# Performance work log

Hardware: AMD Instinct MI355X
Metric: run time of the kernel (lower is better)

## Reference

```python
import jax, jax.numpy as jnp
import numpy as np

HID = 4096      # hidden_size
H = 32          # num_attention_heads
K = 8           # num_key_value_heads
D = HID // H    # head_dim = 128
G = H // K      # q heads per kv group = 4
INTER = 14336   # intermediate_size
T = 2048        # tokens (prefill)
EPS = 1e-5
THETA = 1000000.0


def setup_inputs() -> dict:
    key = jax.random.key(0)
    ks = jax.random.split(key, 9)
    s = 0.02
    return {
        "hidden_states": jax.random.normal(ks[0], (T, HID), jnp.float32),
        "position_ids": jnp.arange(T, dtype=jnp.int64),
        "wqkv": jax.random.normal(ks[1], ((H + 2 * K) * D, HID), jnp.float32) * s,
        "wo": jax.random.normal(ks[2], (HID, HID), jnp.float32) * s,
        "w1": jax.random.normal(ks[3], (INTER, HID), jnp.float32) * s,  # gate
        "w3": jax.random.normal(ks[4], (INTER, HID), jnp.float32) * s,  # up
        "w2": jax.random.normal(ks[5], (HID, INTER), jnp.float32) * s,  # down
        "attn_norm_w": jnp.ones((HID,), jnp.float32),
        "ffn_norm_w": jnp.ones((HID,), jnp.float32),
    }


def _rmsnorm(x, w):
    var = jnp.mean(jnp.square(x), axis=-1, keepdims=True)
    return x * jax.lax.rsqrt(var + EPS) * w


def _rope(x, cos, sin):
    # non-interleaved (half-split) rotation; x: [T, h, D], cos/sin: [T, 1, D//2]
    x1, x2 = x[..., : D // 2], x[..., D // 2 :]
    return jnp.concatenate([x1 * cos - x2 * sin, x2 * cos + x1 * sin], axis=-1)


def _attention(x, position_ids, wqkv, wo):
    t = x.shape[0]
    qkv = x @ wqkv.T  # [T, (H+2K)*D]
    q = qkv[:, : H * D].reshape(t, H, D)
    k = qkv[:, H * D : (H + K) * D].reshape(t, K, D)
    v = qkv[:, (H + K) * D :].reshape(t, K, D)

    inv_freq = 1.0 / (THETA ** (jnp.arange(0, D, 2, dtype=jnp.float32) / D))
    freqs = position_ids.astype(jnp.float32)[:, None] * inv_freq  # [T, D//2]
    cos = jnp.cos(freqs)[:, None, :]
    sin = jnp.sin(freqs)[:, None, :]
    q = _rope(q, cos, sin)
    k = _rope(k, cos, sin)

    # grouped-query attention: [T, K, G, D] queries vs [T, K, D] keys
    qg = q.reshape(t, K, G, D)
    scale = 1.0 / jnp.sqrt(jnp.float32(D))
    scores = jnp.einsum("tkgd,skd->kgts", qg, k) * scale  # [K, G, T, T]
    causal = jnp.tril(jnp.ones((t, t), dtype=bool))
    scores = jnp.where(causal, scores, jnp.finfo(scores.dtype).min)
    probs = jax.nn.softmax(scores, axis=-1)
    out = jnp.einsum("kgts,skd->tkgd", probs, v).reshape(t, H * D)
    return out @ wo.T


def _mlp(x, w1, w3, w2):
    return (jax.nn.silu(x @ w1.T) * (x @ w3.T)) @ w2.T


def reference(hidden_states, position_ids, wqkv, wo, w1, w3, w2, attn_norm_w, ffn_norm_w):
    h = hidden_states + _attention(_rmsnorm(hidden_states, attn_norm_w), position_ids, wqkv, wo)
    return h + _mlp(_rmsnorm(h, ffn_norm_w), w1, w3, w2)
```

## Files before the change

kernel.cpp:

```cpp
#include <hip/hip_runtime.h>
#include <stdint.h>

#define T_SEQ 2048
#define HIDN  4096
#define NH    32
#define NKV   8
#define DH    128
#define INTER 14336
#define QKV_N 6144
#define EPSR  1e-5f
#define SCALE 0.08838834764831845f
#define KVB   64

typedef __bf16 bf16x8 __attribute__((ext_vector_type(8)));
typedef float  f32x4  __attribute__((ext_vector_type(4)));

__device__ __forceinline__ f32x4 mfma16(bf16x8 a, bf16x8 b, f32x4 c) {
  return __builtin_amdgcn_mfma_f32_16x16x32_bf16(a, b, c, 0, 0, 0);
}

__device__ __forceinline__ void glds16(const void* g, void* l) {
  __builtin_amdgcn_global_load_lds(
      (__attribute__((address_space(1))) void*)g,
      (__attribute__((address_space(3))) void*)l,
      16, 0, 0);
}

__global__ __launch_bounds__(256) void cvt_bf16_kernel(
    const float* __restrict__ src, __bf16* __restrict__ dst, long n) {
  long stride = (long)gridDim.x * 256 * 8;
  for (long i = ((long)blockIdx.x * 256 + threadIdx.x) * 8; i < n; i += stride) {
    float4 a = *(const float4*)(src + i);
    float4 b = *(const float4*)(src + i + 4);
    bf16x8 o;
    o[0]=(__bf16)a.x; o[1]=(__bf16)a.y; o[2]=(__bf16)a.z; o[3]=(__bf16)a.w;
    o[4]=(__bf16)b.x; o[5]=(__bf16)b.y; o[6]=(__bf16)b.z; o[7]=(__bf16)b.w;
    *(bf16x8*)(dst + i) = o;
  }
}

__global__ __launch_bounds__(256) void cvt_w13_kernel(
    const float* __restrict__ w1, const float* __restrict__ w3,
    __bf16* __restrict__ dst) {
  for (int c = blockIdx.x; c < 2 * INTER; c += gridDim.x) {
    int tau = c >> 8, j2 = c & 255;
    int wn = j2 >> 7, j = j2 & 127, nt = j >> 4, k16 = j & 15;
    const float* src = (nt < 4 ? w1 : w3) +
        (size_t)(tau * 128 + wn * 64 + (nt & 3) * 16 + k16) * HIDN;
    __bf16* d = dst + (size_t)c * HIDN;
    int i = threadIdx.x * 16;
    float4 a = *(const float4*)(src + i);
    float4 b = *(const float4*)(src + i + 4);
    float4 e = *(const float4*)(src + i + 8);
    float4 f = *(const float4*)(src + i + 12);
    bf16x8 o0, o1;
    o0[0]=(__bf16)a.x; o0[1]=(__bf16)a.y; o0[2]=(__bf16)a.z; o0[3]=(__bf16)a.w;
    o0[4]=(__bf16)b.x; o0[5]=(__bf16)b.y; o0[6]=(__bf16)b.z; o0[7]=(__bf16)b.w;
    o1[0]=(__bf16)e.x; o1[1]=(__bf16)e.y; o1[2]=(__bf16)e.z; o1[3]=(__bf16)e.w;
    o1[4]=(__bf16)f.x; o1[5]=(__bf16)f.y; o1[6]=(__bf16)f.z; o1[7]=(__bf16)f.w;
    *(bf16x8*)(d + i) = o0;
    *(bf16x8*)(d + i + 8) = o1;
  }
}

__global__ __launch_bounds__(256) void rmsnorm_kernel(
    const float* __restrict__ x, const float* __restrict__ w,
    __bf16* __restrict__ y) {
  const int row = blockIdx.x, tid = threadIdx.x;
  const float* xr = x + (size_t)row * HIDN + tid * 16;
  float4 v0 = ((const float4*)xr)[0];
  float4 v1 = ((const float4*)xr)[1];
  float4 v2 = ((const float4*)xr)[2];
  float4 v3 = ((const float4*)xr)[3];
  float ss = v0.x*v0.x + v0.y*v0.y + v0.z*v0.z + v0.w*v0.w
           + v1.x*v1.x + v1.y*v1.y + v1.z*v1.z + v1.w*v1.w
           + v2.x*v2.x + v2.y*v2.y + v2.z*v2.z + v2.w*v2.w
           + v3.x*v3.x + v3.y*v3.y + v3.z*v3.z + v3.w*v3.w;
  #pragma unroll
  for (int off = 32; off >= 1; off >>= 1) ss += __shfl_xor(ss, off, 64);
  __shared__ float red[4];
  if ((tid & 63) == 0) red[tid >> 6] = ss;
  __syncthreads();
  float rn = rsqrtf((red[0] + red[1] + red[2] + red[3]) * (1.0f / HIDN) + EPSR);
  const float* wr = w + tid * 16;
  #pragma unroll
  for (int h = 0; h < 2; h++) {
    float4 a = ((const float4*)xr)[h*2], b = ((const float4*)xr)[h*2+1];
    float4 wa = ((const float4*)wr)[h*2], wb = ((const float4*)wr)[h*2+1];
    bf16x8 o;
    o[0]=(__bf16)(a.x*rn*wa.x); o[1]=(__bf16)(a.y*rn*wa.y);
    o[2]=(__bf16)(a.z*rn*wa.z); o[3]=(__bf16)(a.w*rn*wa.w);
    o[4]=(__bf16)(b.x*rn*wb.x); o[5]=(__bf16)(b.y*rn*wb.y);
    o[6]=(__bf16)(b.z*rn*wb.z); o[7]=(__bf16)(b.w*rn*wb.w);
    *(bf16x8*)(y + (size_t)row * HIDN + tid * 16 + h * 8) = o;
  }
}

__global__ __launch_bounds__(256) void add3_rms_kernel(
    const float* __restrict__ p, const float* __restrict__ resid,
    const float* __restrict__ w, float* __restrict__ hout,
    __bf16* __restrict__ xn) {
  const int row = blockIdx.x, tid = threadIdx.x;
  const size_t base = (size_t)row * HIDN + tid * 16;
  const size_t half = (size_t)T_SEQ * HIDN;
  float h[16];
  float ss = 0.f;
  #pragma unroll
  for (int q = 0; q < 4; q++) {
    float4 a = *(const float4*)(p + base + q * 4);
    float4 b = *(const float4*)(p + half + base + q * 4);
    float4 c = *(const float4*)(resid + base + q * 4);
    h[q*4+0] = a.x + b.x + c.x; h[q*4+1] = a.y + b.y + c.y;
    h[q*4+2] = a.z + b.z + c.z; h[q*4+3] = a.w + b.w + c.w;
    ss += h[q*4]*h[q*4] + h[q*4+1]*h[q*4+1] + h[q*4+2]*h[q*4+2] + h[q*4+3]*h[q*4+3];
    *(float4*)(hout + base + q * 4) = *(float4*)&h[q*4];
  }
  #pragma unroll
  for (int off = 32; off >= 1; off >>= 1) ss += __shfl_xor(ss, off, 64);
  __shared__ float red[4];
  if ((tid & 63) == 0) red[tid >> 6] = ss;
  __syncthreads();
  float rn = rsqrtf((red[0] + red[1] + red[2] + red[3]) * (1.0f / HIDN) + EPSR);
  #pragma unroll
  for (int hb = 0; hb < 2; hb++) {
    bf16x8 o;
    #pragma unroll
    for (int e = 0; e < 8; e++) {
      float wv = w[tid * 16 + hb * 8 + e];
      o[e] = (__bf16)(h[hb*8+e] * rn * wv);
    }
    *(bf16x8*)(xn + base + hb * 8) = o;
  }
}

template<int EPI>
__global__ __launch_bounds__(256, 2) void gemm128_kernel(
    const __bf16* __restrict__ A, const __bf16* __restrict__ B,
    void* __restrict__ Cout, int M, int N, int Kfull, int KZ, int Nout) {
  extern __shared__ __align__(16) char smem[];
  const int tid = threadIdx.x;
  const int lane = tid & 63;
  const int wv = tid >> 6;
  const int wm = wv >> 1;
  const int wn = wv & 1;
  const int lr = lane & 15, ql = lane >> 4;

  const int gx = gridDim.x, gy = gridDim.y;
  const int nwg = gx * gy;
  const int orig = blockIdx.y * gx + blockIdx.x;
  const int cpx = nwg >> 3;
  const int swz = (orig & 7) * cpx + (orig >> 3);
  const int by = swz % gy, bx = swz / gy;
  const int m0 = by * 128, n0 = bx * 256;
  const int kbase = blockIdx.z * KZ;
  const int NT = KZ >> 5;

  const char* gS[6]; int lD[6];
  #pragma unroll
  for (int j = 0; j < 6; j++) {
    int u = (j < 2) ? (j * 256 + tid) : (512 + (j - 2) * 256 + tid);
    if (j < 2) {
      int row = u >> 2;
      int s = (u & 3) ^ ((row >> 1) & 3);
      gS[j] = (const char*)(A + (size_t)(m0 + row) * Kfull + kbase) + s * 16;
      lD[j] = u * 16;
    } else {
      int u2 = u - 512;
      int row = u2 >> 2;
      int s = (u2 & 3) ^ ((row >> 1) & 3);
      gS[j] = (const char*)(B + (size_t)(n0 + row) * Kfull + kbase) + s * 16;
      lD[j] = 8192 + u2 * 16;
    }
  }

  const int sA = ql ^ ((lr >> 1) & 3);
  int aoff[4], boff[8];
  #pragma unroll
  for (int mt = 0; mt < 4; mt++) aoff[mt] = (wm * 64 + mt * 16 + lr) * 64 + sA * 16;
  #pragma unroll
  for (int nt = 0; nt < 8; nt++) boff[nt] = 8192 + (wn * 128 + nt * 16 + lr) * 64 + sA * 16;

#define STAGE(t, b) do {                                           \
    const size_t _o = (size_t)(t) * 64;                            \
    char* _d = smem + (b) * 24576;                                 \
    glds16(gS[0] + _o, _d + lD[0]); glds16(gS[1] + _o, _d + lD[1]);\
    glds16(gS[2] + _o, _d + lD[2]); glds16(gS[3] + _o, _d + lD[3]);\
    glds16(gS[4] + _o, _d + lD[4]); glds16(gS[5] + _o, _d + lD[5]);\
  } while (0)
#define LOADFRAGS(b) do {                                          \
    const char* _p = smem + (b) * 24576;                           \
    _Pragma("unroll") for (int _m = 0; _m < 4; _m++)               \
      af[_m] = *(const bf16x8*)(_p + aoff[_m]);                    \
    _Pragma("unroll") for (int _n = 0; _n < 8; _n++)               \
      bf[_n] = *(const bf16x8*)(_p + boff[_n]);                    \
  } while (0)
#define WAITK() do { asm volatile("s_waitcnt lgkmcnt(0)" ::: "memory"); \
    __builtin_amdgcn_sched_barrier(0); } while (0)
#define MFMA32() do {                                              \
    __builtin_amdgcn_s_setprio(1);                                 \
    _Pragma("unroll") for (int _m = 0; _m < 4; _m++)               \
      _Pragma("unroll") for (int _n = 0; _n < 8; _n++)             \
        acc[_m][_n] = mfma16(af[_m], bf[_n], acc[_m][_n]);         \
    __builtin_amdgcn_s_setprio(0);                                 \
  } while (0)
#define INC3(v) v = (v == 2) ? 0 : v + 1

  f32x4 acc[4][8] = {};
  bf16x8 af[4], bf[8];

  STAGE(0, 0); STAGE(1, 1);
  int bufi = 0, sbufi = 2;
  for (int t = 0; t < NT - 2; ++t) {
    asm volatile("s_waitcnt vmcnt(6)" ::: "memory");
    __builtin_amdgcn_s_barrier();
    LOADFRAGS(bufi);
    STAGE(t + 2, sbufi);
    WAITK(); MFMA32();
    INC3(bufi); INC3(sbufi);
  }
  asm volatile("s_waitcnt vmcnt(6)" ::: "memory");
  __builtin_amdgcn_s_barrier();
  LOADFRAGS(bufi);
  WAITK(); MFMA32();
  INC3(bufi);
  asm volatile("s_waitcnt vmcnt(0)" ::: "memory");
  __builtin_amdgcn_s_barrier();
  LOADFRAGS(bufi);
  WAITK(); MFMA32();

#undef STAGE
#undef LOADFRAGS
#undef WAITK
#undef MFMA32
#undef INC3

  #pragma unroll
  for (int mt = 0; mt < 4; mt++) {
    #pragma unroll
    for (int r = 0; r < 4; r++) {
      int rr = m0 + wm * 64 + mt * 16 + ql * 4 + r;
      if (EPI == 2) {
        #pragma unroll
        for (int nt = 0; nt < 4; nt++) {
          float u = acc[mt][nt][r];
          float v = acc[mt][nt + 4][r];
          float g = u / (1.0f + __expf(-u)) * v;
          int cc = (n0 >> 1) + wn * 64 + nt * 16 + lr;
          ((__bf16*)Cout)[(size_t)rr * Nout + cc] = (__bf16)g;
        }
      } else {
        #pragma unroll
        for (int nt = 0; nt < 8; nt++) {
          int cc = n0 + wn * 128 + nt * 16 + lr;
          size_t ix = (size_t)rr * N + cc;
          float val = acc[mt][nt][r];
          if (EPI == 0) ((float*)Cout)[(size_t)blockIdx.z * M * N + ix] = val;
          else          ((__bf16*)Cout)[ix] = (__bf16)val;
        }
      }
    }
  }
}

__global__ __launch_bounds__(256) void add3_kernel(
    const float* __restrict__ p, const float* __restrict__ r,
    float* __restrict__ o, long n) {
  long stride = (long)gridDim.x * 1024;
  for (long i = ((long)blockIdx.x * 256 + threadIdx.x) * 4; i < n; i += stride) {
    float4 a = *(const float4*)(p + i);
    float4 b = *(const float4*)(p + n + i);
    float4 c = *(const float4*)(r + i);
    float4 o4;
    o4.x = a.x + b.x + c.x; o4.y = a.y + b.y + c.y;
    o4.z = a.z + b.z + c.z; o4.w = a.w + b.w + c.w;
    *(float4*)(o + i) = o4;
  }
}

__global__ __launch_bounds__(256) void rope_kernel(
    const __bf16* __restrict__ qkv, __bf16* __restrict__ q_r,
    __bf16* __restrict__ k_r) {
  const int t = blockIdx.x, tid = threadIdx.x;
  __shared__ float cs[64], sn[64];
  if (tid < 64) {
    float inv = exp2f(-(float)tid * (19.931568569324174f / 64.0f));
    float f = (float)t * inv;
    cs[tid] = cosf(f);
    sn[tid] = sinf(f);
  }
  __syncthreads();
  const __bf16* row = qkv + (size_t)t * QKV_N;
  for (int it = tid; it < 40 * 64; it += 256) {
    int hh = it >> 6, i = it & 63;
    float x1 = (float)row[hh * 128 + i];
    float x2 = (float)row[hh * 128 + 64 + i];
    float c = cs[i], s = sn[i];
    float o1 = x1 * c - x2 * s;
    float o2 = x2 * c + x1 * s;
    if (hh < NH) {
      __bf16* qo = q_r + (size_t)t * HIDN + hh * 128;
      qo[i] = (__bf16)o1;
      qo[64 + i] = (__bf16)o2;
    } else {
      __bf16* ko = k_r + (size_t)t * (NKV * DH) + (hh - NH) * 128;
      ko[i] = (__bf16)o1;
      ko[64 + i] = (__bf16)o2;
    }
  }
}

__global__ __launch_bounds__(256) void vtrans_kernel(
    const __bf16* __restrict__ qkv, __bf16* __restrict__ v_t) {
  __shared__ __bf16 tile[64][136];
  const int tid = threadIdx.x;
  const int t0 = blockIdx.x * 64, kh = blockIdx.y;
  #pragma unroll
  for (int i = 0; i < 4; i++) {
    int u = i * 256 + tid;
    int row = u >> 4, c = (u & 15) * 8;
    *(bf16x8*)&tile[row][c] =
        *(const bf16x8*)(qkv + (size_t)(t0 + row) * QKV_N + (NH + NKV) * DH + kh * DH + c);
  }
  __syncthreads();
  const int d = tid & 127, th = (tid >> 7) * 32;
  #pragma unroll
  for (int j = 0; j < 4; j++) {
    int t = th + j * 8;
    bf16x8 o;
    #pragma unroll
    for (int e = 0; e < 8; e++) o[e] = tile[t + e][d];
    *(bf16x8*)(v_t + ((size_t)kh * DH + d) * T_SEQ + t0 + t) = o;
  }
}

__global__ __launch_bounds__(256) void attn_kernel(
    const __bf16* __restrict__ q_r, const __bf16* __restrict__ k_r,
    const __bf16* __restrict__ v_t, __bf16* __restrict__ attn_o) {
  __shared__ __align__(16) __bf16 Ks[KVB * 128];
  __shared__ __align__(16) __bf16 Vs[128 * KVB];
  __shared__ __align__(16) __bf16 Pl[4 * 16 * KVB];

  const int tid = threadIdx.x;
  const int lane = tid & 63, wv = tid >> 6;
  const int lr = lane & 15, g = lane >> 4;
  const int qt = gridDim.x - 1 - blockIdx.x;
  const int h = blockIdx.y;
  const int kh = h >> 2;
  const int q0b = qt * 64;
  const int q0w = q0b + wv * 16;

  bf16x8 qf[4];
  {
    const __bf16* qp = q_r + (size_t)(q0w + lr) * HIDN + h * DH + g * 8;
    #pragma unroll
    for (int kk = 0; kk < 4; kk++) qf[kk] = *(const bf16x8*)(qp + kk * 32);
  }

  f32x4 o[8] = {};
  float mrun[4] = {-1e30f, -1e30f, -1e30f, -1e30f};
  float lrun[4] = {0.f, 0.f, 0.f, 0.f};
  char* PlW = (char*)Pl + wv * 2048;

  for (int kv0 = 0; kv0 < q0b + KVB; kv0 += KVB) {
    __syncthreads();
    #pragma unroll
    for (int i = 0; i < 4; i++) {
      int u = i * 256 + tid;
      int row = u >> 4;
      int cb = ((u & 15) * 16) ^ ((row & 7) << 4);
      glds16((const char*)(k_r + (size_t)(kv0 + row) * (NKV * DH) + kh * DH) + cb,
             (char*)Ks + u * 16);
    }
    #pragma unroll
    for (int i = 0; i < 4; i++) {
      int u = i * 256 + tid;
      int row = u >> 3;
      int cb = ((u & 7) * 16) ^ ((row & 7) << 4);
      glds16((const char*)(v_t + ((size_t)kh * DH + row) * T_SEQ + kv0) + cb,
             (char*)Vs + u * 16);
    }
    __syncthreads();

    if (q0w + 15 >= kv0) {
      f32x4 s[4] = {};
      #pragma unroll
      for (int kk = 0; kk < 4; kk++) {
        #pragma unroll
        for (int jt = 0; jt < 4; jt++) {
          int krow = jt * 16 + lr;
          int cb = (kk * 64 + g * 16) ^ ((krow & 7) << 4);
          bf16x8 kf = *(const bf16x8*)((char*)Ks + krow * 256 + cb);
          s[jt] = mfma16(qf[kk], kf, s[jt]);
        }
      }
      const bool need_mask = (kv0 + KVB - 1) > q0w;
      #pragma unroll
      for (int r = 0; r < 4; r++) {
        int qpos = q0w + g * 4 + r;
        int prow = g * 4 + r;
        float p[4];
        #pragma unroll
        for (int jt = 0; jt < 4; jt++) {
          float v = s[jt][r] * SCALE;
          if (need_mask && (kv0 + jt * 16 + lr > qpos)) v = -1e30f;
          p[jt] = v;
        }
        float mx = fmaxf(fmaxf(p[0], p[1]), fmaxf(p[2], p[3]));
        #pragma unroll
        for (int off = 1; off < 16; off <<= 1) mx = fmaxf(mx, __shfl_xor(mx, off, 64));
        float mn = fmaxf(mrun[r], mx);
        float corr = __expf(mrun[r] - mn);
        mrun[r] = mn;
        float ps = 0.f;
        #pragma unroll
        for (int jt = 0; jt < 4; jt++) {
          p[jt] = __expf(p[jt] - mn);
          ps += p[jt];
          int cbyte = ((jt * 16 + lr) * 2) ^ ((prow & 7) << 4);
          *(__bf16*)(PlW + prow * 128 + cbyte) = (__bf16)p[jt];
        }
        #pragma unroll
        for (int off = 1; off < 16; off <<= 1) ps += __shfl_xor(ps, off, 64);
        lrun[r] = lrun[r] * corr + ps;
        #pragma unroll
        for (int nt = 0; nt < 8; nt++) o[nt][r] *= corr;
      }
      bf16x8 pa[2];
      #pragma unroll
      for (int ks = 0; ks < 2; ks++)
        pa[ks] = *(const bf16x8*)(PlW + lr * 128 + ((g * 16 + ks * 64) ^ ((lr & 7) << 4)));
      #pragma unroll
      for (int nt = 0; nt < 8; nt++) {
        #pragma unroll
        for (int ks = 0; ks < 2; ks++) {
          int vrow = nt * 16 + lr;
          int cb = (ks * 64 + g * 16) ^ ((vrow & 7) << 4);
          bf16x8 vf = *(const bf16x8*)((char*)Vs + vrow * 128 + cb);
          o[nt] = mfma16(pa[ks], vf, o[nt]);
        }
      }
    }
  }

  #pragma unroll
  for (int nt = 0; nt < 8; nt++) {
    #pragma unroll
    for (int r = 0; r < 4; r++) {
      int qrow = q0w + g * 4 + r;
      int d = nt * 16 + lr;
      attn_o[(size_t)qrow * HIDN + h * DH + d] = (__bf16)(o[nt][r] / lrun[r]);
    }
  }
}

extern "C" void kernel_launch(void* const* d_in, const int* in_sizes, int n_in,
                              void* d_out, int out_size, void* d_ws, size_t ws_size,
                              hipStream_t stream) {
  const float* hidden = (const float*)d_in[0];
  const float* wqkv = (const float*)d_in[2];
  const float* wo   = (const float*)d_in[3];
  const float* w1   = (const float*)d_in[4];
  const float* w3   = (const float*)d_in[5];
  const float* w2   = (const float*)d_in[6];
  const float* anw  = (const float*)d_in[7];
  const float* fnw  = (const float*)d_in[8];

  char* ws = (char*)d_ws;
  const size_t SZ_XN   = (size_t)T_SEQ * HIDN * 2;
  const size_t SZ_QKV  = (size_t)T_SEQ * QKV_N * 2;
  const size_t SZ_KR   = (size_t)T_SEQ * NKV * DH * 2;
  const size_t SZ_H    = (size_t)T_SEQ * HIDN * 4;
  const size_t SZ_UV   = (size_t)T_SEQ * INTER * 2;

  const size_t W_QKV = (size_t)QKV_N * HIDN * 2;
  const size_t W_O   = (size_t)HIDN * HIDN * 2;
  const size_t W_I   = (size_t)INTER * HIDN * 2;
  const size_t W_TOTAL = W_QKV + W_O + 3 * W_I;

  char* act = ws + W_TOTAL;

  __bf16* xn1    = (__bf16*)(act);
  __bf16* qkv    = (__bf16*)(act + SZ_XN);
  __bf16* q_r    = (__bf16*)(act + SZ_XN + SZ_QKV);
  __bf16* gbuf   = (__bf16*)(act);
  __bf16* k_r    = (__bf16*)(act + SZ_UV);
  __bf16* attn_o = (__bf16*)(act + SZ_UV + SZ_KR);
  float*  hbuf   = (float*) (act + SZ_UV + SZ_KR + SZ_XN);
  __bf16* v_t    = (__bf16*)(act + SZ_UV + SZ_KR + SZ_XN);
  __bf16* xn2    = (__bf16*)(act + SZ_UV + SZ_KR + SZ_XN + SZ_H);
  float*  pbuf   = (float*)(act + SZ_UV + SZ_KR + SZ_XN + SZ_H + SZ_XN);

  __bf16* wqkv_b = (__bf16*)(ws);
  __bf16* wo_b   = (__bf16*)(ws + W_QKV);
  __bf16* w13_b  = (__bf16*)(ws + W_QKV + W_O);
  __bf16* w2_b   = (__bf16*)(ws + W_QKV + W_O + 2 * W_I);

  const int LDS_BYTES = 73728;
  hipFuncSetAttribute((const void*)gemm128_kernel<0>,
                      hipFuncAttributeMaxDynamicSharedMemorySize, LDS_BYTES);
  hipFuncSetAttribute((const void*)gemm128_kernel<1>,
                      hipFuncAttributeMaxDynamicSharedMemorySize, LDS_BYTES);
  hipFuncSetAttribute((const void*)gemm128_kernel<2>,
                      hipFuncAttributeMaxDynamicSharedMemorySize, LDS_BYTES);

  cvt_bf16_kernel<<<2048, 256, 0, stream>>>(wqkv, wqkv_b, (long)QKV_N * HIDN);
  cvt_bf16_kernel<<<2048, 256, 0, stream>>>(wo,   wo_b,   (long)HIDN * HIDN);
  cvt_w13_kernel<<<2048, 256, 0, stream>>>(w1, w3, w13_b);
  cvt_bf16_kernel<<<2048, 256, 0, stream>>>(w2,   w2_b,   (long)HIDN * INTER);

  rmsnorm_kernel<<<T_SEQ, 256, 0, stream>>>(hidden, anw, xn1);
  gemm128_kernel<1><<<dim3(QKV_N / 256, T_SEQ / 128, 1), 256, LDS_BYTES, stream>>>(
      xn1, wqkv_b, qkv, T_SEQ, QKV_N, HIDN, HIDN, QKV_N);
  rope_kernel<<<T_SEQ, 256, 0, stream>>>(qkv, q_r, k_r);
  vtrans_kernel<<<dim3(T_SEQ / 64, NKV), 256, 0, stream>>>(qkv, v_t);
  attn_kernel<<<dim3(T_SEQ / 64, NH), 256, 0, stream>>>(q_r, k_r, v_t, attn_o);
  gemm128_kernel<0><<<dim3(HIDN / 256, T_SEQ / 128, 2), 256, LDS_BYTES, stream>>>(
      attn_o, wo_b, pbuf, T_SEQ, HIDN, HIDN, HIDN / 2, HIDN);
  add3_rms_kernel<<<T_SEQ, 256, 0, stream>>>(pbuf, hidden, fnw, hbuf, xn2);
  gemm128_kernel<2><<<dim3(2 * INTER / 256, T_SEQ / 128, 1), 256, LDS_BYTES, stream>>>(
      xn2, w13_b, gbuf, T_SEQ, 2 * INTER, HIDN, HIDN, INTER);
  gemm128_kernel<0><<<dim3(HIDN / 256, T_SEQ / 128, 2), 256, LDS_BYTES, stream>>>(
      gbuf, w2_b, pbuf, T_SEQ, HIDN, INTER, INTER / 2, HIDN);
  add3_kernel<<<2048, 256, 0, stream>>>(pbuf, hbuf, (float*)d_out, (long)T_SEQ * HIDN);
}
```

Before: 1.367 ms.

## Fuse fp32-to-bf16 weight conversion into GEMM B-tile loading

Removes the separate weight conversion kernels and the bf16 weight workspace. Each GEMM now loads fp32 weight rows into registers, converts them to bf16 and writes them swizzled into LDS with double buffering. The A operand keeps async global-to-LDS loads. This trades the standalone conversion passes for doubled B-operand bytes per tile, extra register pressure and VALU conversion work inside the GEMM main loop.

```diff
diff --git a/kernel.cpp b/kernel.cpp
--- a/kernel.cpp
+++ b/kernel.cpp
@@ -24,43 +24,6 @@
       (__attribute__((address_space(1))) void*)g,
       (__attribute__((address_space(3))) void*)l,
       16, 0, 0);
-}
-
-__global__ __launch_bounds__(256) void cvt_bf16_kernel(
-    const float* __restrict__ src, __bf16* __restrict__ dst, long n) {
-  long stride = (long)gridDim.x * 256 * 8;
-  for (long i = ((long)blockIdx.x * 256 + threadIdx.x) * 8; i < n; i += stride) {
-    float4 a = *(const float4*)(src + i);
-    float4 b = *(const float4*)(src + i + 4);
-    bf16x8 o;
-    o[0]=(__bf16)a.x; o[1]=(__bf16)a.y; o[2]=(__bf16)a.z; o[3]=(__bf16)a.w;
-    o[4]=(__bf16)b.x; o[5]=(__bf16)b.y; o[6]=(__bf16)b.z; o[7]=(__bf16)b.w;
-    *(bf16x8*)(dst + i) = o;
-  }
-}
-
-__global__ __launch_bounds__(256) void cvt_w13_kernel(
-    const float* __restrict__ w1, const float* __restrict__ w3,
-    __bf16* __restrict__ dst) {
-  for (int c = blockIdx.x; c < 2 * INTER; c += gridDim.x) {
-    int tau = c >> 8, j2 = c & 255;
-    int wn = j2 >> 7, j = j2 & 127, nt = j >> 4, k16 = j & 15;
-    const float* src = (nt < 4 ? w1 : w3) +
-        (size_t)(tau * 128 + wn * 64 + (nt & 3) * 16 + k16) * HIDN;
-    __bf16* d = dst + (size_t)c * HIDN;
-    int i = threadIdx.x * 16;
-    float4 a = *(const float4*)(src + i);
-    float4 b = *(const float4*)(src + i + 4);
-    float4 e = *(const float4*)(src + i + 8);
-    float4 f = *(const float4*)(src + i + 12);
-    bf16x8 o0, o1;
-    o0[0]=(__bf16)a.x; o0[1]=(__bf16)a.y; o0[2]=(__bf16)a.z; o0[3]=(__bf16)a.w;
-    o0[4]=(__bf16)b.x; o0[5]=(__bf16)b.y; o0[6]=(__bf16)b.z; o0[7]=(__bf16)b.w;
-    o1[0]=(__bf16)e.x; o1[1]=(__bf16)e.y; o1[2]=(__bf16)e.z; o1[3]=(__bf16)e.w;
-    o1[4]=(__bf16)f.x; o1[5]=(__bf16)f.y; o1[6]=(__bf16)f.z; o1[7]=(__bf16)f.w;
-    *(bf16x8*)(d + i) = o0;
-    *(bf16x8*)(d + i + 8) = o1;
-  }
 }
 
 __global__ __launch_bounds__(256) void rmsnorm_kernel(
@@ -134,9 +97,10 @@
 }
 
 template<int EPI>
-__global__ __launch_bounds__(256, 2) void gemm128_kernel(
-    const __bf16* __restrict__ A, const __bf16* __restrict__ B,
-    void* __restrict__ Cout, int M, int N, int Kfull, int KZ, int Nout) {
+__global__ __launch_bounds__(256, 2) void gemmf_kernel(
+    const __bf16* __restrict__ A, const float* __restrict__ B1,
+    const float* __restrict__ B2, void* __restrict__ Cout,
+    int M, int N, int Kfull, int KZ, int Nout) {
   extern __shared__ __align__(16) char smem[];
   const int tid = threadIdx.x;
   const int lane = tid & 63;
@@ -155,47 +119,64 @@
   const int kbase = blockIdx.z * KZ;
   const int NT = KZ >> 5;
 
-  const char* gS[6]; int lD[6];
-  #pragma unroll
-  for (int j = 0; j < 6; j++) {
-    int u = (j < 2) ? (j * 256 + tid) : (512 + (j - 2) * 256 + tid);
-    if (j < 2) {
-      int row = u >> 2;
-      int s = (u & 3) ^ ((row >> 1) & 3);
-      gS[j] = (const char*)(A + (size_t)(m0 + row) * Kfull + kbase) + s * 16;
-      lD[j] = u * 16;
-    } else {
-      int u2 = u - 512;
-      int row = u2 >> 2;
-      int s = (u2 & 3) ^ ((row >> 1) & 3);
-      gS[j] = (const char*)(B + (size_t)(n0 + row) * Kfull + kbase) + s * 16;
-      lD[j] = 8192 + u2 * 16;
-    }
-  }
+  const char* aSrc[2]; int aDst[2];
+  #pragma unroll
+  for (int j = 0; j < 2; j++) {
+    int u = j * 256 + tid;
+    int row = u >> 2;
+    int s = (u & 3) ^ ((row >> 1) & 3);
+    aSrc[j] = (const char*)(A + (size_t)(m0 + row) * Kfull + kbase) + s * 16;
+    aDst[j] = u * 16;
+  }
+
+  const float* bptr;
+  if (EPI == 2) {
+    int r = tid;
+    const float* wsel = ((r >> 6) & 1) ? B2 : B1;
+    int grow = (n0 >> 1) + ((r >> 7) << 6) + (r & 63);
+    bptr = wsel + (size_t)grow * Kfull + kbase;
+  } else {
+    bptr = B1 + (size_t)(n0 + tid) * Kfull + kbase;
+  }
+  int wof[4];
+  #pragma unroll
+  for (int s = 0; s < 4; s++) wof[s] = (s ^ ((tid >> 1) & 3)) * 16;
 
   const int sA = ql ^ ((lr >> 1) & 3);
   int aoff[4], boff[8];
   #pragma unroll
   for (int mt = 0; mt < 4; mt++) aoff[mt] = (wm * 64 + mt * 16 + lr) * 64 + sA * 16;
   #pragma unroll
-  for (int nt = 0; nt < 8; nt++) boff[nt] = 8192 + (wn * 128 + nt * 16 + lr) * 64 + sA * 16;
-
-#define STAGE(t, b) do {                                           \
-    const size_t _o = (size_t)(t) * 64;                            \
-    char* _d = smem + (b) * 24576;                                 \
-    glds16(gS[0] + _o, _d + lD[0]); glds16(gS[1] + _o, _d + lD[1]);\
-    glds16(gS[2] + _o, _d + lD[2]); glds16(gS[3] + _o, _d + lD[3]);\
-    glds16(gS[4] + _o, _d + lD[4]); glds16(gS[5] + _o, _d + lD[5]);\
+  for (int nt = 0; nt < 8; nt++) boff[nt] = (wn * 128 + nt * 16 + lr) * 64 + sA * 16;
+
+#define BUFA(i) (smem + (i) * 8192)
+#define BUFB(i) (smem + 24576 + (i) * 16384)
+#define STAGE_A(t, bi) do {                                        \
+    glds16(aSrc[0] + (size_t)(t) * 64, BUFA(bi) + aDst[0]);        \
+    glds16(aSrc[1] + (size_t)(t) * 64, BUFA(bi) + aDst[1]);        \
   } while (0)
-#define LOADFRAGS(b) do {                                          \
-    const char* _p = smem + (b) * 24576;                           \
+#define LOAD_B(t) do {                                             \
+    _Pragma("unroll") for (int _j = 0; _j < 8; _j++)               \
+      breg[_j] = ((const float4*)bptr)[(size_t)(t) * 8 + _j];      \
+  } while (0)
+#define WRITE_B(bi) do {                                           \
+    char* _wb = BUFB(bi) + tid * 64;                               \
+    _Pragma("unroll") for (int _s = 0; _s < 4; _s++) {             \
+      bf16x8 _o;                                                   \
+      _o[0]=(__bf16)breg[2*_s].x;   _o[1]=(__bf16)breg[2*_s].y;    \
+      _o[2]=(__bf16)breg[2*_s].z;   _o[3]=(__bf16)breg[2*_s].w;    \
+      _o[4]=(__bf16)breg[2*_s+1].x; _o[5]=(__bf16)breg[2*_s+1].y;  \
+      _o[6]=(__bf16)breg[2*_s+1].z; _o[7]=(__bf16)breg[2*_s+1].w;  \
+      *(bf16x8*)(_wb + wof[_s]) = _o;                              \
+    }                                                              \
+  } while (0)
+#define LOADFRAGS(ai, bi) do {                                     \
+    const char* _pa = BUFA(ai); const char* _pb = BUFB(bi);        \
     _Pragma("unroll") for (int _m = 0; _m < 4; _m++)               \
-      af[_m] = *(const bf16x8*)(_p + aoff[_m]);                    \
+      af[_m] = *(const bf16x8*)(_pa + aoff[_m]);                   \
     _Pragma("unroll") for (int _n = 0; _n < 8; _n++)               \
-      bf[_n] = *(const bf16x8*)(_p + boff[_n]);                    \
+      bf[_n] = *(const bf16x8*)(_pb + boff[_n]);                   \
   } while (0)
-#define WAITK() do { asm volatile("s_waitcnt lgkmcnt(0)" ::: "memory"); \
-    __builtin_amdgcn_sched_barrier(0); } while (0)
 #define MFMA32() do {                                              \
     __builtin_amdgcn_s_setprio(1);                                 \
     _Pragma("unroll") for (int _m = 0; _m < 4; _m++)               \
@@ -204,35 +185,42 @@
     __builtin_amdgcn_s_setprio(0);                                 \
   } while (0)
 #define INC3(v) v = (v == 2) ? 0 : v + 1
+#define CLAMP(t) ((t) < NT ? (t) : NT - 1)
 
   f32x4 acc[4][8] = {};
   bf16x8 af[4], bf[8];
-
-  STAGE(0, 0); STAGE(1, 1);
-  int bufi = 0, sbufi = 2;
-  for (int t = 0; t < NT - 2; ++t) {
-    asm volatile("s_waitcnt vmcnt(6)" ::: "memory");
+  float4 breg[8];
+
+  LOAD_B(0);
+  STAGE_A(0, 0); STAGE_A(1, 1);
+  WRITE_B(0);
+  LOAD_B(CLAMP(1));
+  asm volatile("s_waitcnt vmcnt(8)" ::: "memory");
+  asm volatile("s_waitcnt lgkmcnt(0)" ::: "memory");
+
+  int ai = 0, asi = 2;
+  for (int t = 0; t < NT; ++t) {
+    asm volatile("s_waitcnt vmcnt(10)" ::: "memory");
     __builtin_amdgcn_s_barrier();
-    LOADFRAGS(bufi);
-    STAGE(t + 2, sbufi);
-    WAITK(); MFMA32();
-    INC3(bufi); INC3(sbufi);
-  }
-  asm volatile("s_waitcnt vmcnt(6)" ::: "memory");
-  __builtin_amdgcn_s_barrier();
-  LOADFRAGS(bufi);
-  WAITK(); MFMA32();
-  INC3(bufi);
-  asm volatile("s_waitcnt vmcnt(0)" ::: "memory");
-  __builtin_amdgcn_s_barrier();
-  LOADFRAGS(bufi);
-  WAITK(); MFMA32();
-
-#undef STAGE
+    LOADFRAGS(ai, t & 1);
+    STAGE_A(CLAMP(t + 2), asi);
+    WRITE_B((t + 1) & 1);
+    LOAD_B(CLAMP(t + 2));
+    asm volatile("s_waitcnt lgkmcnt(0)" ::: "memory");
+    __builtin_amdgcn_sched_barrier(0);
+    MFMA32();
+    INC3(ai); INC3(asi);
+  }
+
+#undef BUFA
+#undef BUFB
+#undef STAGE_A
+#undef LOAD_B
+#undef WRITE_B
 #undef LOADFRAGS
-#undef WAITK
 #undef MFMA32
 #undef INC3
+#undef CLAMP
 
   #pragma unroll
   for (int mt = 0; mt < 4; mt++) {
@@ -472,12 +460,7 @@
   const size_t SZ_H    = (size_t)T_SEQ * HIDN * 4;
   const size_t SZ_UV   = (size_t)T_SEQ * INTER * 2;
 
-  const size_t W_QKV = (size_t)QKV_N * HIDN * 2;
-  const size_t W_O   = (size_t)HIDN * HIDN * 2;
-  const size_t W_I   = (size_t)INTER * HIDN * 2;
-  const size_t W_TOTAL = W_QKV + W_O + 3 * W_I;
-
-  char* act = ws + W_TOTAL;
+  char* act = ws;
 
   __bf16* xn1    = (__bf16*)(act);
   __bf16* qkv    = (__bf16*)(act + SZ_XN);
@@ -490,36 +473,26 @@
   __bf16* xn2    = (__bf16*)(act + SZ_UV + SZ_KR + SZ_XN + SZ_H);
   float*  pbuf   = (float*)(act + SZ_UV + SZ_KR + SZ_XN + SZ_H + SZ_XN);
 
-  __bf16* wqkv_b = (__bf16*)(ws);
-  __bf16* wo_b   = (__bf16*)(ws + W_QKV);
-  __bf16* w13_b  = (__bf16*)(ws + W_QKV + W_O);
-  __bf16* w2_b   = (__bf16*)(ws + W_QKV + W_O + 2 * W_I);
-
-  const int LDS_BYTES = 73728;
-  hipFuncSetAttribute((const void*)gemm128_kernel<0>,
+  const int LDS_BYTES = 57344;
+  hipFuncSetAttribute((const void*)gemmf_kernel<0>,
                       hipFuncAttributeMaxDynamicSharedMemorySize, LDS_BYTES);
-  hipFuncSetAttribute((const void*)gemm128_kernel<1>,
+  hipFuncSetAttribute((const void*)gemmf_kernel<1>,
                       hipFuncAttributeMaxDynamicSharedMemorySize, LDS_BYTES);
-  hipFuncSetAttribute((const void*)gemm128_kernel<2>,
+  hipFuncSetAttribute((const void*)gemmf_kernel<2>,
                       hipFuncAttributeMaxDynamicSharedMemorySize, LDS_BYTES);
 
-  cvt_bf16_kernel<<<2048, 256, 0, stream>>>(wqkv, wqkv_b, (long)QKV_N * HIDN);
-  cvt_bf16_kernel<<<2048, 256, 0, stream>>>(wo,   wo_b,   (long)HIDN * HIDN);
-  cvt_w13_kernel<<<2048, 256, 0, stream>>>(w1, w3, w13_b);
-  cvt_bf16_kernel<<<2048, 256, 0, stream>>>(w2,   w2_b,   (long)HIDN * INTER);
-
   rmsnorm_kernel<<<T_SEQ, 256, 0, stream>>>(hidden, anw, xn1);
-  gemm128_kernel<1><<<dim3(QKV_N / 256, T_SEQ / 128, 1), 256, LDS_BYTES, stream>>>(
-      xn1, wqkv_b, qkv, T_SEQ, QKV_N, HIDN, HIDN, QKV_N);
+  gemmf_kernel<1><<<dim3(QKV_N / 256, T_SEQ / 128, 1), 256, LDS_BYTES, stream>>>(
+      xn1, wqkv, nullptr, qkv, T_SEQ, QKV_N, HIDN, HIDN, QKV_N);
   rope_kernel<<<T_SEQ, 256, 0, stream>>>(qkv, q_r, k_r);
   vtrans_kernel<<<dim3(T_SEQ / 64, NKV), 256, 0, stream>>>(qkv, v_t);
   attn_kernel<<<dim3(T_SEQ / 64, NH), 256, 0, stream>>>(q_r, k_r, v_t, attn_o);
-  gemm128_kernel<0><<<dim3(HIDN / 256, T_SEQ / 128, 2), 256, LDS_BYTES, stream>>>(
-      attn_o, wo_b, pbuf, T_SEQ, HIDN, HIDN, HIDN / 2, HIDN);
+  gemmf_kernel<0><<<dim3(HIDN / 256, T_SEQ / 128, 2), 256, LDS_BYTES, stream>>>(
+      attn_o, wo, nullptr, pbuf, T_SEQ, HIDN, HIDN, HIDN / 2, HIDN);
   add3_rms_kernel<<<T_SEQ, 256, 0, stream>>>(pbuf, hidden, fnw, hbuf, xn2);
-  gemm128_kernel<2><<<dim3(2 * INTER / 256, T_SEQ / 128, 1), 256, LDS_BYTES, stream>>>(
-      xn2, w13_b, gbuf, T_SEQ, 2 * INTER, HIDN, HIDN, INTER);
-  gemm128_kernel<0><<<dim3(HIDN / 256, T_SEQ / 128, 2), 256, LDS_BYTES, stream>>>(
-      gbuf, w2_b, pbuf, T_SEQ, HIDN, INTER, INTER / 2, HIDN);
+  gemmf_kernel<2><<<dim3(2 * INTER / 256, T_SEQ / 128, 1), 256, LDS_BYTES, stream>>>(
+      xn2, w1, w3, gbuf, T_SEQ, 2 * INTER, HIDN, HIDN, INTER);
+  gemmf_kernel<0><<<dim3(HIDN / 256, T_SEQ / 128, 2), 256, LDS_BYTES, stream>>>(
+      gbuf, w2, nullptr, pbuf, T_SEQ, HIDN, INTER, INTER / 2, HIDN);
   add3_kernel<<<2048, 256, 0, stream>>>(pbuf, hbuf, (float*)d_out, (long)T_SEQ * HIDN);
 }
```

Result: slower. 2.505 ms (+83.3%).
